# Performance work log

Measured on AMD Instinct MI355X. Metric: run time of the kernel, lower is better.

The kernel has to match this reference:

```python
import jax, jax.numpy as jnp
import numpy as np

HS, FF, NH = 1024, 4096, 16
HD = HS // NH
EPS = 1e-5

def _ln(x, g, b):
    m = jnp.mean(x, axis=-1, keepdims=True)
    v = jnp.mean((x - m) ** 2, axis=-1, keepdims=True)
    return (x - m) * jax.lax.rsqrt(v + EPS) * g + b

def setup_inputs() -> dict:
    key = jax.random.key(0)
    ks = jax.random.split(key, 12)
    s = 1.0 / np.sqrt(HS)
    si = 1.0 / np.sqrt(FF)
    d = {
        "hidden_states": jax.random.normal(ks[0], (2, 2048, HS), dtype=jnp.float32),
        "attention_mask": jnp.zeros((2, 1, 1, 2048), dtype=jnp.float32),
        "Wq": jax.random.uniform(ks[1], (HS, HS), minval=-s, maxval=s),
        "bq": jnp.zeros((HS,), jnp.float32),
        "Wk": jax.random.uniform(ks[2], (HS, HS), minval=-s, maxval=s),
        "bk": jnp.zeros((HS,), jnp.float32),
        "Wv": jax.random.uniform(ks[3], (HS, HS), minval=-s, maxval=s),
        "bv": jnp.zeros((HS,), jnp.float32),
        "Wo": jax.random.uniform(ks[4], (HS, HS), minval=-s, maxval=s),
        "bo": jnp.zeros((HS,), jnp.float32),
        "W1": jax.random.uniform(ks[5], (HS, FF), minval=-s, maxval=s),
        "b1": jnp.zeros((FF,), jnp.float32),
        "W2": jax.random.uniform(ks[6], (FF, HS), minval=-si, maxval=si),
        "b2": jnp.zeros((HS,), jnp.float32),
        "ln1_g": jnp.ones((HS,), jnp.float32),
        "ln1_b": jnp.zeros((HS,), jnp.float32),
        "ln2_g": jnp.ones((HS,), jnp.float32),
        "ln2_b": jnp.zeros((HS,), jnp.float32),
    }
    return d

def reference(hidden_states, attention_mask, Wq, bq, Wk, bk, Wv, bv, Wo, bo,
              W1, b1, W2, b2, ln1_g, ln1_b, ln2_g, ln2_b):
    bs, S, _ = hidden_states.shape
    x = hidden_states
    # self-attention (dropout is identity in eval)
    q = (x @ Wq + bq).reshape(bs, S, NH, HD).transpose(0, 2, 1, 3)
    k = (x @ Wk + bk).reshape(bs, S, NH, HD).transpose(0, 2, 1, 3)
    v = (x @ Wv + bv).reshape(bs, S, NH, HD).transpose(0, 2, 1, 3)
    scores = jnp.einsum("bhqd,bhkd->bhqk", q, k) / np.sqrt(HD) + attention_mask
    probs = jax.nn.softmax(scores, axis=-1)
    attn = jnp.einsum("bhqk,bhkd->bhqd", probs, v)
    attn = attn.transpose(0, 2, 1, 3).reshape(bs, S, HS)
    mha = attn @ Wo + bo
    h = _ln(x + mha, ln1_g, ln1_b)
    # FFN
    ff = jax.nn.relu(h @ W1 + b1) @ W2 + b2
    return _ln(h + ff, ln2_g, ln2_b)
```

## Files before the change

kernel.cpp:

```cpp
#include <hip/hip_runtime.h>
#include <hip/hip_bf16.h>

#define HS   1024
#define FF   4096
#define NH   16
#define HD   64
#define SEQ  2048
#define BSZ  2
#define MROWS (BSZ * SEQ)
#define EPS  1e-5f
#define QKV_STRIDE (3 * HS)

typedef float f32x4  __attribute__((ext_vector_type(4)));
typedef short bf16x8 __attribute__((ext_vector_type(8)));

#if __has_builtin(__builtin_amdgcn_exp2f)
#define EXP2(x) __builtin_amdgcn_exp2f(x)
#else
#define EXP2(x) exp2f(x)
#endif

__device__ __forceinline__ unsigned short f2bf(float x) {
  unsigned int u = __float_as_uint(x);
  u += 0x7fffu + ((u >> 16) & 1u);
  return (unsigned short)(u >> 16);
}

__device__ __forceinline__ float bf2f(unsigned short u) {
  return __uint_as_float((unsigned int)u << 16);
}

__device__ __forceinline__ unsigned int pkbf(float a, float b) {
  union { __hip_bfloat162 h; unsigned int u; } x;
  x.h = __float22bfloat162_rn(float2{a, b});
  return x.u;
}

__device__ __forceinline__ void async16(const ushort* g, ushort* lds) {
  __builtin_amdgcn_global_load_lds(
      (const __attribute__((address_space(1))) unsigned int*)g,
      (__attribute__((address_space(3))) unsigned int*)lds, 16, 0, 0);
}

#define BARSB { __builtin_amdgcn_s_barrier(); __builtin_amdgcn_sched_barrier(0); }

#define QUAD(kt, MH, NH)                                                      \
  {                                                                           \
    const ushort* As_ = &smem[(size_t)((kt) & 1) * 32768];                    \
    const ushort* Bs_ = As_ + 16384;                                          \
    bf16x8 af[4][2], bfr[2][2];                                               \
    _Pragma("unroll")                                                         \
    for (int mt = 0; mt < 4; ++mt)                                            \
      _Pragma("unroll")                                                       \
      for (int s = 0; s < 2; ++s) {                                           \
        const int m = wr * 128 + (MH) * 64 + mt * 16 + lr;                    \
        af[mt][s] = *(const bf16x8*)&As_[(size_t)m * 64 +                     \
                                         (((s * 4 + lg) ^ (m & 7)) * 8)];     \
      }                                                                       \
    _Pragma("unroll")                                                         \
    for (int nj = 0; nj < 2; ++nj)                                            \
      _Pragma("unroll")                                                       \
      for (int s = 0; s < 2; ++s) {                                           \
        const int n = wc * 64 + (NH) * 32 + nj * 16 + lr;                     \
        bfr[nj][s] = *(const bf16x8*)&Bs_[(size_t)n * 64 +                    \
                                          (((s * 4 + lg) ^ (n & 7)) * 8)];    \
      }                                                                       \
    __builtin_amdgcn_s_setprio(1);                                            \
    _Pragma("unroll")                                                         \
    for (int s = 0; s < 2; ++s)                                               \
      _Pragma("unroll")                                                       \
      for (int mt = 0; mt < 4; ++mt)                                          \
        _Pragma("unroll")                                                     \
        for (int nj = 0; nj < 2; ++nj)                                        \
          acc[(MH) * 4 + mt][(NH) * 2 + nj] =                                 \
              __builtin_amdgcn_mfma_f32_16x16x32_bf16(                        \
                  af[mt][s], bfr[nj][s], acc[(MH) * 4 + mt][(NH) * 2 + nj],   \
                  0, 0, 0);                                                   \
    __builtin_amdgcn_s_setprio(0);                                            \
  }

template <bool RELU, bool VTRANS, bool PARTIAL>
__global__ __launch_bounds__(512, 2) void gemm8_bf16_kernel(
    const ushort* __restrict__ A, const ushort* __restrict__ Bt,
    const float* __restrict__ bias, ushort* __restrict__ C,
    ushort* __restrict__ VTg,
    float* __restrict__ P0, float* __restrict__ P1, float* __restrict__ P2,
    int M, int N, int K, int kSplit)
{
  __shared__ ushort smem[65536];
  const int tid = threadIdx.x;
  const int wv = tid >> 6, ln = tid & 63;
  const int wr = wv >> 2, wc = wv & 3;
  const int lr = ln & 15, lg = ln >> 4;
  const int rr = ln >> 3, cc = ln & 7;

  const unsigned nxy = gridDim.x * gridDim.y;
  unsigned id = blockIdx.y * gridDim.x + blockIdx.x;
  id = (id & 7) * (nxy >> 3) + (id >> 3);
  const int bn = id % gridDim.x, bm = id / gridDim.x;

  int kBeg = 0, kEnd = K;
  if (PARTIAL) {
    kBeg = blockIdx.z * kSplit;
    kEnd = kBeg + kSplit; if (kEnd > K) kEnd = K;
  }
  const int jBeg = kBeg >> 7, jEnd = kEnd >> 7;

  f32x4 acc[8][4];
#pragma unroll
  for (int i = 0; i < 8; ++i)
#pragma unroll
    for (int j = 0; j < 4; ++j) acc[i][j] = (f32x4){0.f, 0.f, 0.f, 0.f};

  auto stA = [&](int kt, int h) {
#pragma unroll
    for (int u = 0; u < 2; ++u) {
      const int tt = h + u * 2;
      const int R = tt * 64 + wv * 8 + rr;
      async16(A + (size_t)(bm * 256 + R) * K + kt * 64 + ((cc ^ (R & 7)) * 8),
              &smem[(size_t)(kt & 1) * 32768 + (size_t)(tt * 64 + wv * 8) * 64]);
    }
  };
  auto stB = [&](int kt, int h) {
#pragma unroll
    for (int u = 0; u < 2; ++u) {
      const int tt = h * 2 + u;
      const int R = tt * 64 + wv * 8 + rr;
      async16(Bt + (size_t)(bn * 256 + R) * K + kt * 64 + ((cc ^ (R & 7)) * 8),
              &smem[(size_t)(kt & 1) * 32768 + 16384 + (size_t)(tt * 64 + wv * 8) * 64]);
    }
  };

  const int tP = 2 * jBeg;
  stA(tP, 0); stA(tP, 1); stB(tP, 0); stB(tP, 1); stA(tP + 1, 0);

  for (int j = jBeg; j < jEnd; ++j) {
    const int t0 = 2 * j, t1 = t0 + 1;
    const bool nx = (j + 1 < jEnd);
    BARSB;
    stA(t1, 1);
    asm volatile("s_waitcnt vmcnt(4)" ::: "memory");
    BARSB;
    QUAD(t0, 0, 0);
    BARSB; stB(t1, 0); QUAD(t0, 0, 1);
    BARSB; if (nx) stA(t0 + 2, 0); QUAD(t0, 1, 0);
    BARSB; stB(t1, 1); QUAD(t0, 1, 1);
    BARSB;
    if (nx) {
      stA(t0 + 2, 1);
      asm volatile("s_waitcnt vmcnt(2)" ::: "memory");
    } else {
      asm volatile("s_waitcnt vmcnt(0)" ::: "memory");
    }
    BARSB;
    QUAD(t1, 0, 0);
    BARSB; if (nx) stB(t0 + 2, 0); QUAD(t1, 0, 1);
    BARSB; if (nx) stB(t0 + 2, 1); QUAD(t1, 1, 0);
    BARSB; if (nx) stA(t0 + 3, 0); QUAD(t1, 1, 1);
  }

  const int gm0 = bm * 256 + wr * 128;
  const int gn0 = bn * 256 + wc * 64;

  if (PARTIAL) {
    float* Cp = (blockIdx.z == 0) ? P0 : (blockIdx.z == 1) ? P1 : P2;
#pragma unroll
    for (int i = 0; i < 8; ++i) {
#pragma unroll
      for (int r = 0; r < 4; ++r) {
        const size_t row = (size_t)(gm0 + i * 16 + lg * 4 + r);
#pragma unroll
        for (int j = 0; j < 4; ++j)
          Cp[row * N + gn0 + j * 16 + lr] = acc[i][j][r];
      }
    }
    return;
  }

  float bs4[4];
#pragma unroll
  for (int j = 0; j < 4; ++j) bs4[j] = bias[gn0 + j * 16 + lr];

  if (VTRANS && gn0 >= 2 * HS) {
#pragma unroll
    for (int i = 0; i < 8; ++i) {
#pragma unroll
      for (int j = 0; j < 4; ++j) {
        const int col = gn0 - 2 * HS + j * 16 + lr;
        const int rowb = gm0 + i * 16 + lg * 4;
        const int bb = rowb >> 11;
        const int seq = rowb & (SEQ - 1);
        ushort4 o;
        o.x = f2bf(acc[i][j][0] + bs4[j]);
        o.y = f2bf(acc[i][j][1] + bs4[j]);
        o.z = f2bf(acc[i][j][2] + bs4[j]);
        o.w = f2bf(acc[i][j][3] + bs4[j]);
        *(ushort4*)&VTg[((size_t)(bb * NH + (col >> 6)) * 64 + (col & 63)) * SEQ + seq] = o;
      }
    }
  } else {
#pragma unroll
    for (int i = 0; i < 8; ++i) {
#pragma unroll
      for (int r = 0; r < 4; ++r) {
        const size_t row = (size_t)(gm0 + i * 16 + lg * 4 + r);
#pragma unroll
        for (int j = 0; j < 4; ++j) {
          float val = acc[i][j][r] + bs4[j];
          if (RELU) val = fmaxf(val, 0.f);
          C[row * N + gn0 + j * 16 + lr] = f2bf(val);
        }
      }
    }
  }
}

template <int TBM, int TBN, bool RELU, bool OUT_BF16, bool PARTIAL>
__global__ __launch_bounds__(256) void gemm_bf16_kernel(
    const ushort* __restrict__ A, const ushort* __restrict__ Bt,
    const float* __restrict__ bias, void* __restrict__ Cout,
    int M, int N, int K, int kLen, size_t zstride)
{
  constexpr int MI = TBM / 32;
  constexpr int NJ = TBN / 32;
  __shared__ ushort As[TBM * 64];
  __shared__ ushort Bs[TBN * 64];

  const int tid = threadIdx.x;
  const int wv = tid >> 6, ln = tid & 63;

  const unsigned nxy = gridDim.x * gridDim.y;
  unsigned id = blockIdx.y * gridDim.x + blockIdx.x;
  id = (id & 7) * (nxy >> 3) + (id >> 3);
  const int bn = id % gridDim.x, bm = id / gridDim.x;

  const int lr = ln & 15;
  const int lg = ln >> 4;
  const int mrow_base = (wv >> 1) * (TBM / 2);
  const int ncol_base = (wv & 1) * (TBN / 2);

  f32x4 acc[MI][NJ];
#pragma unroll
  for (int i = 0; i < MI; ++i)
#pragma unroll
    for (int j = 0; j < NJ; ++j) acc[i][j] = (f32x4){0.f, 0.f, 0.f, 0.f};

  const int rr = ln >> 3, cc = ln & 7;
  const int kBeg = blockIdx.z * kLen, kEnd = kBeg + kLen;

  for (int k0 = kBeg; k0 < kEnd; k0 += 64) {
    __syncthreads();
#pragma unroll
    for (int t = 0; t < TBM / 32; ++t) {
      const int R = wv * (TBM / 4) + t * 8 + rr;
      const int c = cc ^ (R & 7);
      async16(A + (size_t)(bm * TBM + R) * K + k0 + c * 8,
              &As[(size_t)(wv * (TBM / 4) + t * 8) * 64]);
    }
#pragma unroll
    for (int t = 0; t < TBN / 32; ++t) {
      const int R = wv * (TBN / 4) + t * 8 + rr;
      const int c = cc ^ (R & 7);
      async16(Bt + (size_t)(bn * TBN + R) * K + k0 + c * 8,
              &Bs[(size_t)(wv * (TBN / 4) + t * 8) * 64]);
    }
    __syncthreads();

#pragma unroll
    for (int s = 0; s < 2; ++s) {
      bf16x8 a[MI], b[NJ];
#pragma unroll
      for (int i = 0; i < MI; ++i) {
        const int m = mrow_base + i * 16 + lr;
        a[i] = *(const bf16x8*)&As[(size_t)m * 64 + (((s * 4 + lg) ^ (m & 7)) * 8)];
      }
#pragma unroll
      for (int j = 0; j < NJ; ++j) {
        const int n = ncol_base + j * 16 + lr;
        b[j] = *(const bf16x8*)&Bs[(size_t)n * 64 + (((s * 4 + lg) ^ (n & 7)) * 8)];
      }
#pragma unroll
      for (int i = 0; i < MI; ++i)
#pragma unroll
        for (int j = 0; j < NJ; ++j)
          acc[i][j] = __builtin_amdgcn_mfma_f32_16x16x32_bf16(a[i], b[j], acc[i][j], 0, 0, 0);
    }
  }

  const int gm0 = bm * TBM + mrow_base;
  const int gn0 = bn * TBN + ncol_base;

  if (PARTIAL) {
    float* Cp = (float*)Cout + (size_t)blockIdx.z * zstride;
#pragma unroll
    for (int i = 0; i < MI; ++i)
#pragma unroll
      for (int r = 0; r < 4; ++r) {
        const size_t row = (size_t)(gm0 + i * 16 + lg * 4 + r);
#pragma unroll
        for (int j = 0; j < NJ; ++j)
          Cp[row * N + gn0 + j * 16 + lr] = acc[i][j][r];
      }
  } else {
    float bs4[NJ];
#pragma unroll
    for (int j = 0; j < NJ; ++j) bs4[j] = bias[gn0 + j * 16 + lr];
    float* Cf = (float*)Cout;
    ushort* Cb = (ushort*)Cout;
#pragma unroll
    for (int i = 0; i < MI; ++i) {
#pragma unroll
      for (int r = 0; r < 4; ++r) {
        const size_t row = (size_t)(gm0 + i * 16 + lg * 4 + r);
#pragma unroll
        for (int j = 0; j < NJ; ++j) {
          float val = acc[i][j][r] + bs4[j];
          if (RELU) val = fmaxf(val, 0.f);
          const size_t idx = row * N + gn0 + j * 16 + lr;
          if (OUT_BF16) Cb[idx] = f2bf(val);
          else          Cf[idx] = val;
        }
      }
    }
  }
}

__device__ __forceinline__ void transpose_tile(
    const float* __restrict__ W, ushort* __restrict__ Wt,
    int K, int N, int n0, int k0, int tid, ushort (*T)[72])
{
#pragma unroll
  for (int t = 0; t < 4; ++t) {
    const int r = t * 16 + (tid >> 4);
    const int c = (tid & 15) * 4;
    const float4 w = *(const float4*)&W[(size_t)(k0 + r) * N + n0 + c];
    T[c + 0][r] = f2bf(w.x); T[c + 1][r] = f2bf(w.y);
    T[c + 2][r] = f2bf(w.z); T[c + 3][r] = f2bf(w.w);
  }
  __syncthreads();
#pragma unroll
  for (int t = 0; t < 4; ++t) {
    const int n = t * 16 + (tid >> 4);
    const int kc = (tid & 15) * 4;
    ushort4 o;
    o.x = T[n][kc]; o.y = T[n][kc + 1]; o.z = T[n][kc + 2]; o.w = T[n][kc + 3];
    *(ushort4*)&Wt[(size_t)(n0 + n) * K + k0 + kc] = o;
  }
}

__global__ __launch_bounds__(256) void prep_kernel(
    const float* __restrict__ Wq, const float* __restrict__ Wk,
    const float* __restrict__ Wv, const float* __restrict__ Wo,
    const float* __restrict__ W1, const float* __restrict__ W2,
    const float* __restrict__ bq, const float* __restrict__ bk,
    const float* __restrict__ bv, const float* __restrict__ x,
    const float* __restrict__ mask,
    ushort* __restrict__ Wqkvt, ushort* __restrict__ Wot,
    ushort* __restrict__ W1t, ushort* __restrict__ W2t,
    float* __restrict__ bqkv, ushort* __restrict__ xb,
    float* __restrict__ maskL2)
{
  __shared__ ushort T[64][72];
  const int b = blockIdx.x, tid = threadIdx.x;
  const size_t M1 = 1024 * 1024;
  if (b < 1024) {
    const int w = b >> 8, l = b & 255;
    const int n0 = (l & 15) * 64, k0 = (l >> 4) * 64;
    const float* src = (w == 0) ? Wq : (w == 1) ? Wk : (w == 2) ? Wv : Wo;
    ushort* dst = (w < 3) ? (Wqkvt + (size_t)w * M1) : Wot;
    transpose_tile(src, dst, HS, HS, n0, k0, tid, T);
  } else if (b < 2048) {
    const int l = b - 1024;
    transpose_tile(W1, W1t, HS, FF, (l & 63) * 64, (l >> 6) * 64, tid, T);
  } else if (b < 3072) {
    const int l = b - 2048;
    transpose_tile(W2, W2t, FF, HS, (l & 15) * 64, (l >> 4) * 64, tid, T);
  } else if (b < 5120) {
    const size_t base = (size_t)(b - 3072) * 2048 + tid * 8;
    const float4 v0 = *(const float4*)&x[base];
    const float4 v1 = *(const float4*)&x[base + 4];
    ushort4 o0, o1;
    o0.x = f2bf(v0.x); o0.y = f2bf(v0.y); o0.z = f2bf(v0.z); o0.w = f2bf(v0.w);
    o1.x = f2bf(v1.x); o1.y = f2bf(v1.y); o1.z = f2bf(v1.z); o1.w = f2bf(v1.w);
    *(ushort4*)&xb[base] = o0;
    *(ushort4*)&xb[base + 4] = o1;
  } else {
#pragma unroll
    for (int t = 0; t < 12; ++t) {
      const int i = t * 256 + tid;
      bqkv[i] = (i < HS) ? bq[i] : (i < 2 * HS) ? bk[i - HS] : bv[i - 2 * HS];
    }
#pragma unroll
    for (int t = 0; t < 16; ++t) {
      const int i = t * 256 + tid;
      maskL2[i] = mask[i] * 1.44269504f;
    }
  }
}

__global__ __launch_bounds__(512, 2) void attention_mfma_kernel(
    const ushort* __restrict__ Qb, const ushort* __restrict__ Kb,
    const ushort* __restrict__ VTg, const float* __restrict__ maskL2,
    ushort* __restrict__ O)
{
  __shared__ ushort smem[69632];
  float* mL = (float*)(smem + 65536);

  const int tid = threadIdx.x;
  const int wv = tid >> 6, ln = tid & 63;
  const int c = ln & 15, g = ln >> 4;

  const unsigned d0 = blockIdx.x + 8u * (blockIdx.y + 16u * blockIdx.z);
  const unsigned w0 = (d0 & 7) * 32 + (d0 >> 3);
  const int qt = w0 & 7;
  const int hh = (w0 >> 3) & 15;
  const int b  = w0 >> 7;

  const int bh = b * NH + hh;
  const size_t row0 = (size_t)b * SEQ + (size_t)qt * 256;
  const int ch = hh * HD;
  const int wq0 = wv * 32;

  bf16x8 qf[2][2];
#pragma unroll
  for (int nt = 0; nt < 2; ++nt)
#pragma unroll
    for (int s = 0; s < 2; ++s)
      qf[nt][s] = *(const bf16x8*)&Qb[(row0 + wq0 + nt * 16 + c) * QKV_STRIDE + ch + s * 32 + g * 8];

  const float* mrow = maskL2 + (size_t)b * SEQ;
  async16((const ushort*)(mrow + wv * 256 + ln * 4), (ushort*)(mL + wv * 256));

  const int rr = ln >> 3, cc = ln & 7;
  const int r4 = ln >> 4, sc = ln & 15;

  auto stage = [&](int kb, int bsel) {
    ushort* Ks  = smem + bsel * 16384;
    ushort* VTs = Ks + 8192;
    const size_t krow0 = (size_t)b * SEQ + (size_t)kb * 128;
#pragma unroll
    for (int t = 0; t < 2; ++t) {
      const int r = wv * 16 + t * 8 + rr;
      async16(Kb + (krow0 + r) * QKV_STRIDE + ch + ((cc ^ (r & 7)) * 8),
              &Ks[(size_t)(wv * 16 + t * 8) * 64]);
    }
#pragma unroll
    for (int t = 0; t < 2; ++t) {
      const int d = wv * 8 + t * 4 + r4;
      const int srcc = (sc & 8) | ((sc & 7) ^ (d & 7));
      async16(VTg + ((size_t)bh * 64 + d) * SEQ + kb * 128 + srcc * 8,
              &VTs[(size_t)(wv * 8 + t * 4) * 128]);
    }
  };

  f32x4 ao[4][2];
#pragma unroll
  for (int i = 0; i < 4; ++i) { ao[i][0] = (f32x4){0,0,0,0}; ao[i][1] = (f32x4){0,0,0,0}; }
  f32x4 aol[2];
  aol[0] = (f32x4){0,0,0,0}; aol[1] = (f32x4){0,0,0,0};
  const short oneb = (short)0x3F80;
  const bf16x8 ones = (bf16x8){oneb, oneb, oneb, oneb, oneb, oneb, oneb, oneb};

  stage(0, 0);
  stage(1, 1);

  constexpr int NT = SEQ / 128;
  for (int kb = 0; kb < NT; ++kb) {
    const int cur = kb & 3;
    if (kb + 2 < NT) stage(kb + 2, (kb + 2) & 3);
    if (kb + 2 < NT)      asm volatile("s_waitcnt vmcnt(8)" ::: "memory");
    else if (kb + 1 < NT) asm volatile("s_waitcnt vmcnt(4)" ::: "memory");
    else                  asm volatile("s_waitcnt vmcnt(0)" ::: "memory");
    __builtin_amdgcn_s_barrier();
    __builtin_amdgcn_sched_barrier(0);

    ushort* Ks  = smem + cur * 16384;
    ushort* VTs = Ks + 8192;

    f32x4 asA[4][2], asB[4][2];
#pragma unroll
    for (int i = 0; i < 4; ++i) {
      asA[i][0] = (f32x4){0,0,0,0}; asA[i][1] = (f32x4){0,0,0,0};
      asB[i][0] = (f32x4){0,0,0,0}; asB[i][1] = (f32x4){0,0,0,0};
    }
    __builtin_amdgcn_s_setprio(1);
#pragma unroll
    for (int s = 0; s < 2; ++s) {
#pragma unroll
      for (int mt = 0; mt < 4; ++mt) {
        const int key = mt * 16 + c;
        const bf16x8 kf = *(const bf16x8*)&Ks[(size_t)key * 64 + (((s * 4 + g) ^ (key & 7)) * 8)];
#pragma unroll
        for (int nt = 0; nt < 2; ++nt)
          asA[mt][nt] = __builtin_amdgcn_mfma_f32_16x16x32_bf16(kf, qf[nt][s], asA[mt][nt], 0, 0, 0);
      }
    }
#pragma unroll
    for (int s = 0; s < 2; ++s) {
#pragma unroll
      for (int mt = 0; mt < 4; ++mt) {
        const int key = (mt + 4) * 16 + c;
        const bf16x8 kf = *(const bf16x8*)&Ks[(size_t)key * 64 + (((s * 4 + g) ^ (key & 7)) * 8)];
#pragma unroll
        for (int nt = 0; nt < 2; ++nt)
          asB[mt][nt] = __builtin_amdgcn_mfma_f32_16x16x32_bf16(kf, qf[nt][s], asB[mt][nt], 0, 0, 0);
      }
    }
    __builtin_amdgcn_s_setprio(0);

#pragma unroll
    for (int mt = 0; mt < 4; ++mt) {
      const float4 mk = *(const float4*)&mL[kb * 128 + mt * 16 + g * 4];
      const float mka[4] = {mk.x, mk.y, mk.z, mk.w};
#pragma unroll
      for (int nt = 0; nt < 2; ++nt) {
#pragma unroll
        for (int r = 0; r < 4; ++r)
          asA[mt][nt][r] = EXP2(fmaf(asA[mt][nt][r], 0.18033688f, mka[r]));
      }
    }

#pragma unroll
    for (int s = 0; s < 2; ++s) {
      bf16x8 pf[2];
#pragma unroll
      for (int nt = 0; nt < 2; ++nt) {
        const unsigned A0 = pkbf(asA[2 * s][nt][0], asA[2 * s][nt][1]);
        const unsigned A1 = pkbf(asA[2 * s][nt][2], asA[2 * s][nt][3]);
        const unsigned B0 = pkbf(asA[2 * s + 1][nt][0], asA[2 * s + 1][nt][1]);
        const unsigned B1 = pkbf(asA[2 * s + 1][nt][2], asA[2 * s + 1][nt][3]);
        auto x0 = __builtin_amdgcn_permlane32_swap(A0, B0, false, false);
        auto x1 = __builtin_amdgcn_permlane32_swap(A1, B1, false, false);
        auto y0 = __builtin_amdgcn_permlane16_swap(x0[0], x0[1], false, false);
        auto y1 = __builtin_amdgcn_permlane16_swap(x1[0], x1[1], false, false);
        union { unsigned w[4]; bf16x8 v; } u;
        u.w[0] = y0[0]; u.w[1] = y1[0]; u.w[2] = y0[1]; u.w[3] = y1[1];
        pf[nt] = u.v;
      }
      __builtin_amdgcn_s_setprio(1);
#pragma unroll
      for (int mt = 0; mt < 4; ++mt) {
        const int d = mt * 16 + c;
        const int k = s * 4 + g;
        const int vslot = (k & 8) | ((k & 7) ^ (d & 7));
        const bf16x8 vf = *(const bf16x8*)&VTs[(size_t)d * 128 + vslot * 8];
#pragma unroll
        for (int nt = 0; nt < 2; ++nt)
          ao[mt][nt] = __builtin_amdgcn_mfma_f32_16x16x32_bf16(vf, pf[nt], ao[mt][nt], 0, 0, 0);
      }
#pragma unroll
      for (int nt = 0; nt < 2; ++nt)
        aol[nt] = __builtin_amdgcn_mfma_f32_16x16x32_bf16(ones, pf[nt], aol[nt], 0, 0, 0);
      __builtin_amdgcn_s_setprio(0);
    }

#pragma unroll
    for (int mt = 0; mt < 4; ++mt) {
      const float4 mk = *(const float4*)&mL[kb * 128 + (mt + 4) * 16 + g * 4];
      const float mka[4] = {mk.x, mk.y, mk.z, mk.w};
#pragma unroll
      for (int nt = 0; nt < 2; ++nt) {
#pragma unroll
        for (int r = 0; r < 4; ++r)
          asB[mt][nt][r] = EXP2(fmaf(asB[mt][nt][r], 0.18033688f, mka[r]));
      }
    }

#pragma unroll
    for (int s = 2; s < 4; ++s) {
      const int sb = s - 2;
      bf16x8 pf[2];
#pragma unroll
      for (int nt = 0; nt < 2; ++nt) {
        const unsigned A0 = pkbf(asB[2 * sb][nt][0], asB[2 * sb][nt][1]);
        const unsigned A1 = pkbf(asB[2 * sb][nt][2], asB[2 * sb][nt][3]);
        const unsigned B0 = pkbf(asB[2 * sb + 1][nt][0], asB[2 * sb + 1][nt][1]);
        const unsigned B1 = pkbf(asB[2 * sb + 1][nt][2], asB[2 * sb + 1][nt][3]);
        auto x0 = __builtin_amdgcn_permlane32_swap(A0, B0, false, false);
        auto x1 = __builtin_amdgcn_permlane32_swap(A1, B1, false, false);
        auto y0 = __builtin_amdgcn_permlane16_swap(x0[0], x0[1], false, false);
        auto y1 = __builtin_amdgcn_permlane16_swap(x1[0], x1[1], false, false);
        union { unsigned w[4]; bf16x8 v; } u;
        u.w[0] = y0[0]; u.w[1] = y1[0]; u.w[2] = y0[1]; u.w[3] = y1[1];
        pf[nt] = u.v;
      }
      __builtin_amdgcn_s_setprio(1);
#pragma unroll
      for (int mt = 0; mt < 4; ++mt) {
        const int d = mt * 16 + c;
        const int k = s * 4 + g;
        const int vslot = (k & 8) | ((k & 7) ^ (d & 7));
        const bf16x8 vf = *(const bf16x8*)&VTs[(size_t)d * 128 + vslot * 8];
#pragma unroll
        for (int nt = 0; nt < 2; ++nt)
          ao[mt][nt] = __builtin_amdgcn_mfma_f32_16x16x32_bf16(vf, pf[nt], ao[mt][nt], 0, 0, 0);
      }
#pragma unroll
      for (int nt = 0; nt < 2; ++nt)
        aol[nt] = __builtin_amdgcn_mfma_f32_16x16x32_bf16(ones, pf[nt], aol[nt], 0, 0, 0);
      __builtin_amdgcn_s_setprio(0);
    }
  }

  __syncthreads();
  ushort* OL = smem;
#pragma unroll
  for (int nt = 0; nt < 2; ++nt) {
    const float inv = 1.f / aol[nt][0];
    const int q = wq0 + nt * 16 + c;
#pragma unroll
    for (int mt = 0; mt < 4; ++mt) {
      const int d = mt * 16 + g * 4;
      uint2 w;
      w.x = pkbf(ao[mt][nt][0] * inv, ao[mt][nt][1] * inv);
      w.y = pkbf(ao[mt][nt][2] * inv, ao[mt][nt][3] * inv);
      *(uint2*)&OL[q * 72 + d] = w;
    }
  }
  __syncthreads();
#pragma unroll
  for (int it = 0; it < 4; ++it) {
    const int unit = it * 512 + tid;
    const int q = unit >> 3, sg = unit & 7;
    const uint4 w = *(const uint4*)&OL[q * 72 + sg * 8];
    *(uint4*)&O[(row0 + q) * HS + ch + sg * 8] = w;
  }
}

__global__ __launch_bounds__(256) void add_ln_red3_kernel(
    const float* __restrict__ P0, const float* __restrict__ P1,
    const float* __restrict__ P2,
    const float* __restrict__ bias, const float* __restrict__ X,
    const float* __restrict__ g, const float* __restrict__ b,
    float* __restrict__ out)
{
  const int row = blockIdx.x;
  const int tid = threadIdx.x;
  const size_t base = (size_t)row * HS + tid * 4;
  const float4 p0 = *(const float4*)&P0[base];
  const float4 p1 = *(const float4*)&P1[base];
  const float4 p2 = *(const float4*)&P2[base];
  const float4 bi = *(const float4*)&bias[tid * 4];
  const float4 xv = *(const float4*)&X[base];
  float4 v;
  v.x = xv.x + p0.x + p1.x + p2.x + bi.x;
  v.y = xv.y + p0.y + p1.y + p2.y + bi.y;
  v.z = xv.z + p0.z + p1.z + p2.z + bi.z;
  v.w = xv.w + p0.w + p1.w + p2.w + bi.w;
  float s1 = v.x + v.y + v.z + v.w;
  float s2 = v.x * v.x + v.y * v.y + v.z * v.z + v.w * v.w;
#pragma unroll
  for (int off = 32; off > 0; off >>= 1) {
    s1 += __shfl_down(s1, off, 64);
    s2 += __shfl_down(s2, off, 64);
  }
  __shared__ float red[8];
  __shared__ float stat[2];
  const int wid = tid >> 6;
  if ((tid & 63) == 0) { red[wid] = s1; red[4 + wid] = s2; }
  __syncthreads();
  if (tid == 0) {
    const float t1 = red[0] + red[1] + red[2] + red[3];
    const float t2 = red[4] + red[5] + red[6] + red[7];
    const float mean = t1 * (1.f / HS);
    const float var = t2 * (1.f / HS) - mean * mean;
    stat[0] = mean;
    stat[1] = rsqrtf(var + EPS);
  }
  __syncthreads();
  const float mean = stat[0], rstd = stat[1];
  const float4 gv = *(const float4*)&g[tid * 4];
  const float4 bv = *(const float4*)&b[tid * 4];
  float4 r;
  r.x = (v.x - mean) * rstd * gv.x + bv.x;
  r.y = (v.y - mean) * rstd * gv.y + bv.y;
  r.z = (v.z - mean) * rstd * gv.z + bv.z;
  r.w = (v.w - mean) * rstd * gv.w + bv.w;
  *(float4*)&out[base] = r;
}

__global__ __launch_bounds__(256) void add_ln_bf16_kernel(
    const ushort* __restrict__ Pb, const float* __restrict__ X,
    const float* __restrict__ g, const float* __restrict__ b,
    float* __restrict__ out, ushort* __restrict__ outb)
{
  const int row = blockIdx.x;
  const int tid = threadIdx.x;
  const size_t base = (size_t)row * HS + tid * 4;
  const ushort4 pb = *(const ushort4*)&Pb[base];
  const float4 xv = *(const float4*)&X[base];
  float4 v;
  v.x = xv.x + bf2f(pb.x);
  v.y = xv.y + bf2f(pb.y);
  v.z = xv.z + bf2f(pb.z);
  v.w = xv.w + bf2f(pb.w);
  float s1 = v.x + v.y + v.z + v.w;
  float s2 = v.x * v.x + v.y * v.y + v.z * v.z + v.w * v.w;
#pragma unroll
  for (int off = 32; off > 0; off >>= 1) {
    s1 += __shfl_down(s1, off, 64);
    s2 += __shfl_down(s2, off, 64);
  }
  __shared__ float red[8];
  __shared__ float stat[2];
  const int wid = tid >> 6;
  if ((tid & 63) == 0) { red[wid] = s1; red[4 + wid] = s2; }
  __syncthreads();
  if (tid == 0) {
    const float t1 = red[0] + red[1] + red[2] + red[3];
    const float t2 = red[4] + red[5] + red[6] + red[7];
    const float mean = t1 * (1.f / HS);
    const float var = t2 * (1.f / HS) - mean * mean;
    stat[0] = mean;
    stat[1] = rsqrtf(var + EPS);
  }
  __syncthreads();
  const float mean = stat[0], rstd = stat[1];
  const float4 gv = *(const float4*)&g[tid * 4];
  const float4 bv = *(const float4*)&b[tid * 4];
  float4 r;
  r.x = (v.x - mean) * rstd * gv.x + bv.x;
  r.y = (v.y - mean) * rstd * gv.y + bv.y;
  r.z = (v.z - mean) * rstd * gv.z + bv.z;
  r.w = (v.w - mean) * rstd * gv.w + bv.w;
  *(float4*)&out[base] = r;
  ushort4 o;
  o.x = f2bf(r.x); o.y = f2bf(r.y); o.z = f2bf(r.z); o.w = f2bf(r.w);
  *(ushort4*)&outb[base] = o;
}

extern "C" void kernel_launch(void* const* d_in, const int* in_sizes, int n_in,
                              void* d_out, int out_size, void* d_ws, size_t ws_size,
                              hipStream_t stream)
{
  const float* x    = (const float*)d_in[0];
  const float* mask = (const float*)d_in[1];
  const float* Wq   = (const float*)d_in[2];  const float* bq  = (const float*)d_in[3];
  const float* Wk   = (const float*)d_in[4];  const float* bk  = (const float*)d_in[5];
  const float* Wv   = (const float*)d_in[6];  const float* bv  = (const float*)d_in[7];
  const float* Wo   = (const float*)d_in[8];  const float* bo  = (const float*)d_in[9];
  const float* W1   = (const float*)d_in[10]; const float* b1  = (const float*)d_in[11];
  const float* W2   = (const float*)d_in[12]; const float* b2  = (const float*)d_in[13];
  const float* g1   = (const float*)d_in[14]; const float* be1 = (const float*)d_in[15];
  const float* g2   = (const float*)d_in[16]; const float* be2 = (const float*)d_in[17];
  float* out = (float*)d_out;

  ushort* wsu = (ushort*)d_ws;
  const size_t M1 = 1024 * 1024;

  ushort* Wqkvt = wsu;
  ushort* Wot   = wsu + 3 * M1;
  ushort* W1t   = wsu + 4 * M1;
  ushort* W2t   = wsu + 8 * M1;
  float*  bqkv  = (float*)(wsu + 12 * M1);
  float*  maskL2= (float*)(wsu + 12 * M1 + 8192);
  ushort* xb    = wsu + 13 * M1;
  ushort* qkvb  = wsu + 17 * M1;
  ushort* VTg   = wsu + 29 * M1;
  ushort* attnb = wsu + 33 * M1;
  ushort* mhab  = wsu + 13 * M1;
  float*  h     = (float*)(wsu + 29 * M1);
  ushort* hb    = wsu + 37 * M1;
  ushort* ff1o  = wsu + 13 * M1;
  float*  ff2P0 = (float*)wsu;
  float*  ff2P1 = (float*)(wsu + 37 * M1);
  float*  ff2P2 = out;

  const dim3 blk(256);

  prep_kernel<<<dim3(5121), blk, 0, stream>>>(
      Wq, Wk, Wv, Wo, W1, W2, bq, bk, bv, x, mask,
      Wqkvt, Wot, W1t, W2t, bqkv, xb, maskL2);

  gemm8_bf16_kernel<false, true, false><<<dim3(12, 16), dim3(512), 0, stream>>>(
      xb, Wqkvt, bqkv, qkvb, VTg, nullptr, nullptr, nullptr, MROWS, 3 * HS, HS, 0);

  attention_mfma_kernel<<<dim3(SEQ / 256, NH, BSZ), dim3(512), 0, stream>>>(
      qkvb, qkvb + HS, VTg, maskL2, attnb);

  gemm_bf16_kernel<64, 128, false, true, false><<<dim3(8, 64), blk, 0, stream>>>(
      attnb, Wot, bo, mhab, MROWS, HS, HS, HS, 0);
  add_ln_bf16_kernel<<<dim3(MROWS), blk, 0, stream>>>(
      mhab, x, g1, be1, h, hb);

  gemm8_bf16_kernel<true, false, false><<<dim3(16, 16), dim3(512), 0, stream>>>(
      hb, W1t, b1, ff1o, nullptr, nullptr, nullptr, nullptr, MROWS, FF, HS, 0);

  gemm8_bf16_kernel<false, false, true><<<dim3(4, 16, 3), dim3(512), 0, stream>>>(
      ff1o, W2t, nullptr, nullptr, nullptr, ff2P0, ff2P1, ff2P2,
      MROWS, HS, FF, 1408);
  add_ln_red3_kernel<<<dim3(MROWS), blk, 0, stream>>>(
      ff2P0, ff2P1, ff2P2, b2, h, g2, be2, out);
}
```

Measured before the change: 332.7 us.

## Use 256-key KV tiles with double buffering in attention kernel

Changes the attention inner loop from 128-key tiles in a 4-slot ring (prefetch two ahead) to 256-key tiles double-buffered, with the next tile staged right after the barrier. Each tile is now processed as four 64-key sub-blocks, so fewer loop iterations and barriers are needed per head. In exchange, every iteration waits with vmcnt(0) and prefetches only one tile ahead, which may expose more load latency. The 256-key tile also changes the V-transpose swizzle layout.

New measurement: 337.9 us. No clear change (+1.5%).

```diff
diff --git a/kernel.cpp b/kernel.cpp
--- a/kernel.cpp
+++ b/kernel.cpp
@@ -432,24 +432,24 @@
   async16((const ushort*)(mrow + wv * 256 + ln * 4), (ushort*)(mL + wv * 256));
 
   const int rr = ln >> 3, cc = ln & 7;
-  const int r4 = ln >> 4, sc = ln & 15;
+  const int dsub = ln >> 5, sc2 = ln & 31;
 
   auto stage = [&](int kb, int bsel) {
-    ushort* Ks  = smem + bsel * 16384;
-    ushort* VTs = Ks + 8192;
-    const size_t krow0 = (size_t)b * SEQ + (size_t)kb * 128;
-#pragma unroll
-    for (int t = 0; t < 2; ++t) {
-      const int r = wv * 16 + t * 8 + rr;
+    ushort* Ks  = smem + bsel * 32768;
+    ushort* VTs = Ks + 16384;
+    const size_t krow0 = (size_t)b * SEQ + (size_t)kb * 256;
+#pragma unroll
+    for (int t = 0; t < 4; ++t) {
+      const int r = wv * 32 + t * 8 + rr;
       async16(Kb + (krow0 + r) * QKV_STRIDE + ch + ((cc ^ (r & 7)) * 8),
-              &Ks[(size_t)(wv * 16 + t * 8) * 64]);
-    }
-#pragma unroll
-    for (int t = 0; t < 2; ++t) {
-      const int d = wv * 8 + t * 4 + r4;
-      const int srcc = (sc & 8) | ((sc & 7) ^ (d & 7));
-      async16(VTg + ((size_t)bh * 64 + d) * SEQ + kb * 128 + srcc * 8,
-              &VTs[(size_t)(wv * 8 + t * 4) * 128]);
+              &Ks[(size_t)(wv * 32 + t * 8) * 64]);
+    }
+#pragma unroll
+    for (int t = 0; t < 4; ++t) {
+      const int d = wv * 8 + t * 2 + dsub;
+      const int srcc = (sc2 & 24) | ((sc2 & 7) ^ (d & 7));
+      async16(VTg + ((size_t)bh * 64 + d) * SEQ + kb * 256 + srcc * 8,
+              &VTs[(size_t)(wv * 8 + t * 2) * 256]);
     }
   };
 
@@ -462,143 +462,84 @@
   const bf16x8 ones = (bf16x8){oneb, oneb, oneb, oneb, oneb, oneb, oneb, oneb};
 
   stage(0, 0);
-  stage(1, 1);
-
-  constexpr int NT = SEQ / 128;
+
+  constexpr int NT = SEQ / 256;
   for (int kb = 0; kb < NT; ++kb) {
-    const int cur = kb & 3;
-    if (kb + 2 < NT) stage(kb + 2, (kb + 2) & 3);
-    if (kb + 2 < NT)      asm volatile("s_waitcnt vmcnt(8)" ::: "memory");
-    else if (kb + 1 < NT) asm volatile("s_waitcnt vmcnt(4)" ::: "memory");
-    else                  asm volatile("s_waitcnt vmcnt(0)" ::: "memory");
+    const int cur = kb & 1;
+    asm volatile("s_waitcnt vmcnt(0)" ::: "memory");
     __builtin_amdgcn_s_barrier();
     __builtin_amdgcn_sched_barrier(0);
-
-    ushort* Ks  = smem + cur * 16384;
-    ushort* VTs = Ks + 8192;
-
-    f32x4 asA[4][2], asB[4][2];
-#pragma unroll
-    for (int i = 0; i < 4; ++i) {
-      asA[i][0] = (f32x4){0,0,0,0}; asA[i][1] = (f32x4){0,0,0,0};
-      asB[i][0] = (f32x4){0,0,0,0}; asB[i][1] = (f32x4){0,0,0,0};
-    }
-    __builtin_amdgcn_s_setprio(1);
-#pragma unroll
-    for (int s = 0; s < 2; ++s) {
+    if (kb + 1 < NT) stage(kb + 1, cur ^ 1);
+
+    ushort* Ks  = smem + cur * 32768;
+    ushort* VTs = Ks + 16384;
+
+#pragma unroll
+    for (int qd = 0; qd < 4; ++qd) {
+      f32x4 as_[4][2];
+#pragma unroll
+      for (int i = 0; i < 4; ++i) { as_[i][0] = (f32x4){0,0,0,0}; as_[i][1] = (f32x4){0,0,0,0}; }
+
+      __builtin_amdgcn_s_setprio(1);
+#pragma unroll
+      for (int s = 0; s < 2; ++s) {
+#pragma unroll
+        for (int mt = 0; mt < 4; ++mt) {
+          const int key = qd * 64 + mt * 16 + c;
+          const bf16x8 kf = *(const bf16x8*)&Ks[(size_t)key * 64 + (((s * 4 + g) ^ (key & 7)) * 8)];
+#pragma unroll
+          for (int nt = 0; nt < 2; ++nt)
+            as_[mt][nt] = __builtin_amdgcn_mfma_f32_16x16x32_bf16(kf, qf[nt][s], as_[mt][nt], 0, 0, 0);
+        }
+      }
+      __builtin_amdgcn_s_setprio(0);
+
 #pragma unroll
       for (int mt = 0; mt < 4; ++mt) {
-        const int key = mt * 16 + c;
-        const bf16x8 kf = *(const bf16x8*)&Ks[(size_t)key * 64 + (((s * 4 + g) ^ (key & 7)) * 8)];
+        const float4 mk = *(const float4*)&mL[kb * 256 + qd * 64 + mt * 16 + g * 4];
+        const float mka[4] = {mk.x, mk.y, mk.z, mk.w};
+#pragma unroll
+        for (int nt = 0; nt < 2; ++nt) {
+#pragma unroll
+          for (int r = 0; r < 4; ++r)
+            as_[mt][nt][r] = EXP2(fmaf(as_[mt][nt][r], 0.18033688f, mka[r]));
+        }
+      }
+
+#pragma unroll
+      for (int s2 = 0; s2 < 2; ++s2) {
+        const int s = qd * 2 + s2;
+        bf16x8 pf[2];
+#pragma unroll
+        for (int nt = 0; nt < 2; ++nt) {
+          const unsigned A0 = pkbf(as_[2 * s2][nt][0], as_[2 * s2][nt][1]);
+          const unsigned A1 = pkbf(as_[2 * s2][nt][2], as_[2 * s2][nt][3]);
+          const unsigned B0 = pkbf(as_[2 * s2 + 1][nt][0], as_[2 * s2 + 1][nt][1]);
+          const unsigned B1 = pkbf(as_[2 * s2 + 1][nt][2], as_[2 * s2 + 1][nt][3]);
+          auto x0 = __builtin_amdgcn_permlane32_swap(A0, B0, false, false);
+          auto x1 = __builtin_amdgcn_permlane32_swap(A1, B1, false, false);
+          auto y0 = __builtin_amdgcn_permlane16_swap(x0[0], x0[1], false, false);
+          auto y1 = __builtin_amdgcn_permlane16_swap(x1[0], x1[1], false, false);
+          union { unsigned w[4]; bf16x8 v; } u;
+          u.w[0] = y0[0]; u.w[1] = y1[0]; u.w[2] = y0[1]; u.w[3] = y1[1];
+          pf[nt] = u.v;
+        }
+        __builtin_amdgcn_s_setprio(1);
+#pragma unroll
+        for (int mt = 0; mt < 4; ++mt) {
+          const int d = mt * 16 + c;
+          const int k = s * 4 + g;
+          const int vslot = (k & 24) | ((k & 7) ^ (d & 7));
+          const bf16x8 vf = *(const bf16x8*)&VTs[(size_t)d * 256 + vslot * 8];
+#pragma unroll
+          for (int nt = 0; nt < 2; ++nt)
+            ao[mt][nt] = __builtin_amdgcn_mfma_f32_16x16x32_bf16(vf, pf[nt], ao[mt][nt], 0, 0, 0);
+        }
 #pragma unroll
         for (int nt = 0; nt < 2; ++nt)
-          asA[mt][nt] = __builtin_amdgcn_mfma_f32_16x16x32_bf16(kf, qf[nt][s], asA[mt][nt], 0, 0, 0);
-      }
-    }
-#pragma unroll
-    for (int s = 0; s < 2; ++s) {
-#pragma unroll
-      for (int mt = 0; mt < 4; ++mt) {
-        const int key = (mt + 4) * 16 + c;
-        const bf16x8 kf = *(const bf16x8*)&Ks[(size_t)key * 64 + (((s * 4 + g) ^ (key & 7)) * 8)];
-#pragma unroll
-        for (int nt = 0; nt < 2; ++nt)
-          asB[mt][nt] = __builtin_amdgcn_mfma_f32_16x16x32_bf16(kf, qf[nt][s], asB[mt][nt], 0, 0, 0);
-      }
-    }
-    __builtin_amdgcn_s_setprio(0);
-
-#pragma unroll
-    for (int mt = 0; mt < 4; ++mt) {
-      const float4 mk = *(const float4*)&mL[kb * 128 + mt * 16 + g * 4];
-      const float mka[4] = {mk.x, mk.y, mk.z, mk.w};
-#pragma unroll
-      for (int nt = 0; nt < 2; ++nt) {
-#pragma unroll
-        for (int r = 0; r < 4; ++r)
-          asA[mt][nt][r] = EXP2(fmaf(asA[mt][nt][r], 0.18033688f, mka[r]));
-      }
-    }
-
-#pragma unroll
-    for (int s = 0; s < 2; ++s) {
-      bf16x8 pf[2];
-#pragma unroll
-      for (int nt = 0; nt < 2; ++nt) {
-        const unsigned A0 = pkbf(asA[2 * s][nt][0], asA[2 * s][nt][1]);
-        const unsigned A1 = pkbf(asA[2 * s][nt][2], asA[2 * s][nt][3]);
-        const unsigned B0 = pkbf(asA[2 * s + 1][nt][0], asA[2 * s + 1][nt][1]);
-        const unsigned B1 = pkbf(asA[2 * s + 1][nt][2], asA[2 * s + 1][nt][3]);
-        auto x0 = __builtin_amdgcn_permlane32_swap(A0, B0, false, false);
-        auto x1 = __builtin_amdgcn_permlane32_swap(A1, B1, false, false);
-        auto y0 = __builtin_amdgcn_permlane16_swap(x0[0], x0[1], false, false);
-        auto y1 = __builtin_amdgcn_permlane16_swap(x1[0], x1[1], false, false);
-        union { unsigned w[4]; bf16x8 v; } u;
-        u.w[0] = y0[0]; u.w[1] = y1[0]; u.w[2] = y0[1]; u.w[3] = y1[1];
-        pf[nt] = u.v;
-      }
-      __builtin_amdgcn_s_setprio(1);
-#pragma unroll
-      for (int mt = 0; mt < 4; ++mt) {
-        const int d = mt * 16 + c;
-        const int k = s * 4 + g;
-        const int vslot = (k & 8) | ((k & 7) ^ (d & 7));
-        const bf16x8 vf = *(const bf16x8*)&VTs[(size_t)d * 128 + vslot * 8];
-#pragma unroll
-        for (int nt = 0; nt < 2; ++nt)
-          ao[mt][nt] = __builtin_amdgcn_mfma_f32_16x16x32_bf16(vf, pf[nt], ao[mt][nt], 0, 0, 0);
-      }
-#pragma unroll
-      for (int nt = 0; nt < 2; ++nt)
-        aol[nt] = __builtin_amdgcn_mfma_f32_16x16x32_bf16(ones, pf[nt], aol[nt], 0, 0, 0);
-      __builtin_amdgcn_s_setprio(0);
-    }
-
-#pragma unroll
-    for (int mt = 0; mt < 4; ++mt) {
-      const float4 mk = *(const float4*)&mL[kb * 128 + (mt + 4) * 16 + g * 4];
-      const float mka[4] = {mk.x, mk.y, mk.z, mk.w};
-#pragma unroll
-      for (int nt = 0; nt < 2; ++nt) {
-#pragma unroll
-        for (int r = 0; r < 4; ++r)
-          asB[mt][nt][r] = EXP2(fmaf(asB[mt][nt][r], 0.18033688f, mka[r]));
-      }
-    }
-
-#pragma unroll
-    for (int s = 2; s < 4; ++s) {
-      const int sb = s - 2;
-      bf16x8 pf[2];
-#pragma unroll
-      for (int nt = 0; nt < 2; ++nt) {
-        const unsigned A0 = pkbf(asB[2 * sb][nt][0], asB[2 * sb][nt][1]);
-        const unsigned A1 = pkbf(asB[2 * sb][nt][2], asB[2 * sb][nt][3]);
-        const unsigned B0 = pkbf(asB[2 * sb + 1][nt][0], asB[2 * sb + 1][nt][1]);
-        const unsigned B1 = pkbf(asB[2 * sb + 1][nt][2], asB[2 * sb + 1][nt][3]);
-        auto x0 = __builtin_amdgcn_permlane32_swap(A0, B0, false, false);
-        auto x1 = __builtin_amdgcn_permlane32_swap(A1, B1, false, false);
-        auto y0 = __builtin_amdgcn_permlane16_swap(x0[0], x0[1], false, false);
-        auto y1 = __builtin_amdgcn_permlane16_swap(x1[0], x1[1], false, false);
-        union { unsigned w[4]; bf16x8 v; } u;
-        u.w[0] = y0[0]; u.w[1] = y1[0]; u.w[2] = y0[1]; u.w[3] = y1[1];
-        pf[nt] = u.v;
-      }
-      __builtin_amdgcn_s_setprio(1);
-#pragma unroll
-      for (int mt = 0; mt < 4; ++mt) {
-        const int d = mt * 16 + c;
-        const int k = s * 4 + g;
-        const int vslot = (k & 8) | ((k & 7) ^ (d & 7));
-        const bf16x8 vf = *(const bf16x8*)&VTs[(size_t)d * 128 + vslot * 8];
-#pragma unroll
-        for (int nt = 0; nt < 2; ++nt)
-          ao[mt][nt] = __builtin_amdgcn_mfma_f32_16x16x32_bf16(vf, pf[nt], ao[mt][nt], 0, 0, 0);
-      }
-#pragma unroll
-      for (int nt = 0; nt < 2; ++nt)
-        aol[nt] = __builtin_amdgcn_mfma_f32_16x16x32_bf16(ones, pf[nt], aol[nt], 0, 0, 0);
-      __builtin_amdgcn_s_setprio(0);
+          aol[nt] = __builtin_amdgcn_mfma_f32_16x16x32_bf16(ones, pf[nt], aol[nt], 0, 0, 0);
+        __builtin_amdgcn_s_setprio(0);
+      }
     }
   }
 
```
